# Kernel tuning notes

Measured on AMD Instinct MI355X. Metric: run time of the kernel, lower is better.

The kernel has to match this reference:

```python
import jax, jax.numpy as jnp
import numpy as np

HEADS = 4
ALPHA = 0.2  # leaky relu negative slope


def setup_inputs() -> dict:
    key = jax.random.key(0)
    ks = jax.random.split(key, 8)
    N, Fin, Fout = 4096, 512, 256
    return {
        "h": jax.random.normal(ks[0], (N, Fin), dtype=jnp.float32),
        "adj": jax.random.randint(ks[1], (N, N), 0, 2, dtype=jnp.int32),
        "W": jax.random.normal(ks[2], (Fin, Fout), dtype=jnp.float32) * (Fin ** -0.5),
        "Wl_w": jax.random.normal(ks[3], (Fout, Fout), dtype=jnp.float32) * (Fout ** -0.5),
        "Wl_b": jax.random.normal(ks[4], (Fout,), dtype=jnp.float32) * 0.02,
        "Wqkv_w": jax.random.normal(ks[5], (3 * Fout, Fout), dtype=jnp.float32) * (Fout ** -0.5),
        "Wqkv_b": jax.random.normal(ks[6], (3 * Fout,), dtype=jnp.float32) * 0.02,
        "a": jax.random.normal(ks[7], (2 * Fout, 1), dtype=jnp.float32) * (Fout ** -0.5),
    }


def reference(h, adj, W, Wl_w, Wl_b, Wqkv_w, Wqkv_b, a):
    N = h.shape[0]
    Fout = W.shape[1]
    d = Fout // HEADS
    scale = Fout ** -0.5  # note: original scales by out_features^-0.5, not head_dim

    Wh = h @ W                      # [N, Fout]
    Wh = Wh @ Wl_w.T + Wl_b         # to_linear

    qkv = Wh @ Wqkv_w.T + Wqkv_b    # [N, 3*Fout]
    q, k, v = jnp.split(qkv, 3, axis=-1)
    to_heads = lambda t: t.reshape(N, HEADS, d).transpose(1, 0, 2)  # [H, N, d]
    q, k, v = to_heads(q), to_heads(k), to_heads(v)

    dots = jax.nn.softmax(jnp.einsum('hid,hjd->hij', q, k) * scale, axis=-1)  # [H,N,N]
    Wh0 = jnp.einsum('hij,hjd->hid', dots, v)            # [H, N, d]
    Wh0 = Wh0.transpose(1, 0, 2).reshape(N, Fout)        # i (h d)
    Wh0 = jax.nn.softmax(Wh0, axis=-1)

    # GAT score decomposed: e_ij = leakyrelu(Wh_i . a1 + Wh_j . a2)
    a1 = a[:Fout, 0]
    a2 = a[Fout:, 0]
    e = jax.nn.leaky_relu((Wh @ a1)[:, None] + (Wh @ a2)[None, :], negative_slope=ALPHA)

    dsum = dots.sum(axis=0)                              # [N, N]
    neg = jnp.float32(-9e15)
    attention = jnp.where(adj > 0, e + dsum, neg)
    attention = jax.nn.softmax(attention, axis=1)
    # dropout p=0.0 / eval mode -> identity

    h_prime = attention @ Wh + Wh0
    return jax.nn.elu(h_prime)  # concat=True
```

## Files before the change

kernel.cpp:

```cpp
#include <hip/hip_runtime.h>

typedef float  f32x4 __attribute__((ext_vector_type(4)));
typedef short  s16x8 __attribute__((ext_vector_type(8)));
typedef unsigned short u16x8 __attribute__((ext_vector_type(8)));

#define NROWS 4096
#define FOUT  256
#define ALPHA_LR 0.2f
#define SCALE 0.0625f
#define NEGV  -9.0e15f

static __device__ __forceinline__ unsigned short bf16_rne(float x) {
    unsigned u = __float_as_uint(x);
    u += 0x7fffu + ((u >> 16) & 1u);
    return (unsigned short)(u >> 16);
}
static __device__ __forceinline__ unsigned short bf16_trunc(float x) {
    return (unsigned short)(__float_as_uint(x) >> 16);
}
static __device__ __forceinline__ float bf2f(unsigned short h) {
    return __uint_as_float(((unsigned)h) << 16);
}
static __device__ __forceinline__ float wmax16(float v) {
#pragma unroll
    for (int o = 8; o; o >>= 1) v = fmaxf(v, __shfl_xor(v, o, 16));
    return v;
}
static __device__ __forceinline__ float wsum16(float v) {
#pragma unroll
    for (int o = 8; o; o >>= 1) v += __shfl_xor(v, o, 16);
    return v;
}
static __device__ __forceinline__ float wmax32(float v) {
#pragma unroll
    for (int o = 16; o; o >>= 1) v = fmaxf(v, __shfl_xor(v, o, 32));
    return v;
}
static __device__ __forceinline__ float wsum32(float v) {
#pragma unroll
    for (int o = 16; o; o >>= 1) v += __shfl_xor(v, o, 32);
    return v;
}

__global__ __launch_bounds__(256) void wprep(
    const float* __restrict__ W, const float* __restrict__ Wq,
    unsigned short* __restrict__ Whi, unsigned short* __restrict__ Wlo,
    unsigned short* __restrict__ Qhi, unsigned short* __restrict__ Qlo)
{
    int i = blockIdx.x * 256 + threadIdx.x;
    if (i < 131072) {
        float v = W[i];
        unsigned short hh = bf16_trunc(v);
        Whi[i] = hh; Wlo[i] = bf16_rne(v - bf2f(hh));
    }
    if (i < 196608) {
        float v = Wq[i];
        unsigned short hh = bf16_trunc(v);
        Qhi[i] = hh; Qlo[i] = bf16_rne(v - bf2f(hh));
    }
}

template <int EPI, bool BIAS>
__global__ __launch_bounds__(256) void gemm_mfma(
    const float* __restrict__ A,
    const unsigned short* __restrict__ Bhi, const unsigned short* __restrict__ Blo,
    const float* __restrict__ bias,
    float* __restrict__ C, unsigned short* __restrict__ o0,
    unsigned short* __restrict__ o1, unsigned short* __restrict__ o2,
    int M, int Nn, int K)
{
    __shared__ unsigned short Ah[64][40];
    __shared__ unsigned short Al[64][40];
    __shared__ unsigned short Bh[64][40];
    __shared__ unsigned short Bl[64][40];

    const int tid = threadIdx.x;
    const int w = tid >> 6;
    const int ln = tid & 63;
    const int l15 = ln & 15;
    const int lhi = ln >> 4;
    const int bm = blockIdx.y * 64;
    const int bn = blockIdx.x * 64;
    const int sm = tid >> 2;
    const int sk = (tid & 3) * 8;

    f32x4 acc[4];
#pragma unroll
    for (int cf = 0; cf < 4; ++cf) acc[cf] = (f32x4){0.f, 0.f, 0.f, 0.f};

    const float* arow = &A[(size_t)(bm + sm) * K];
    const unsigned short* bhrow = &Bhi[(size_t)(bn + sm) * K];
    const unsigned short* blrow = &Blo[(size_t)(bn + sm) * K];

    float4 a0r = *(const float4*)(arow + sk);
    float4 a1r = *(const float4*)(arow + sk + 4);
    uint4 bhr = *(const uint4*)(bhrow + sk);
    uint4 blr = *(const uint4*)(blrow + sk);

    for (int k0 = 0; k0 < K; k0 += 32) {
        float vv[8] = {a0r.x, a0r.y, a0r.z, a0r.w, a1r.x, a1r.y, a1r.z, a1r.w};
        unsigned hp[4], lp[4];
#pragma unroll
        for (int q = 0; q < 4; ++q) {
            unsigned short h0 = bf16_trunc(vv[q * 2]);
            unsigned short h1 = bf16_trunc(vv[q * 2 + 1]);
            unsigned short l0 = bf16_rne(vv[q * 2] - bf2f(h0));
            unsigned short l1 = bf16_rne(vv[q * 2 + 1] - bf2f(h1));
            hp[q] = (unsigned)h0 | ((unsigned)h1 << 16);
            lp[q] = (unsigned)l0 | ((unsigned)l1 << 16);
        }
        __syncthreads();
        *(uint4*)&Ah[sm][sk] = make_uint4(hp[0], hp[1], hp[2], hp[3]);
        *(uint4*)&Al[sm][sk] = make_uint4(lp[0], lp[1], lp[2], lp[3]);
        *(uint4*)&Bh[sm][sk] = bhr;
        *(uint4*)&Bl[sm][sk] = blr;
        const int kn = (k0 + 32 < K) ? k0 + 32 : 0;
        a0r = *(const float4*)(arow + kn + sk);
        a1r = *(const float4*)(arow + kn + sk + 4);
        bhr = *(const uint4*)(bhrow + kn + sk);
        blr = *(const uint4*)(blrow + kn + sk);
        __syncthreads();
        s16x8 ah = *(const s16x8*)&Ah[w * 16 + l15][lhi * 8];
        s16x8 al2 = *(const s16x8*)&Al[w * 16 + l15][lhi * 8];
        __builtin_amdgcn_s_setprio(1);
#pragma unroll
        for (int cf = 0; cf < 4; ++cf) {
            s16x8 bh = *(const s16x8*)&Bh[cf * 16 + l15][lhi * 8];
            s16x8 bl = *(const s16x8*)&Bl[cf * 16 + l15][lhi * 8];
            acc[cf] = __builtin_amdgcn_mfma_f32_16x16x32_bf16(ah, bh, acc[cf], 0, 0, 0);
            acc[cf] = __builtin_amdgcn_mfma_f32_16x16x32_bf16(ah, bl, acc[cf], 0, 0, 0);
            acc[cf] = __builtin_amdgcn_mfma_f32_16x16x32_bf16(al2, bh, acc[cf], 0, 0, 0);
        }
        __builtin_amdgcn_s_setprio(0);
    }

#pragma unroll
    for (int cf = 0; cf < 4; ++cf) {
        const int col = bn + cf * 16 + l15;
        float bv = BIAS ? bias[col] : 0.0f;
#pragma unroll
        for (int r = 0; r < 4; ++r) {
            const int row = bm + w * 16 + lhi * 4 + r;
            float v = acc[cf][r] + bv;
            if (EPI == 1) {
                C[(size_t)row * Nn + col] = v;
                o0[(size_t)col * NROWS + row] = bf16_rne(v);
            } else if (EPI == 2) {
                if (col < 256)      o0[(size_t)row * 256 + col] = bf16_rne(v);
                else if (col < 512) o1[(size_t)row * 256 + (col - 256)] = bf16_rne(v);
                else                o2[(size_t)(col - 512) * NROWS + row] = bf16_rne(v);
            } else {
                unsigned short hh = bf16_trunc(v);
                o0[(size_t)row * Nn + col] = hh;
                o1[(size_t)row * Nn + col] = bf16_rne(v - bf2f(hh));
            }
        }
    }
}

__global__ __launch_bounds__(256) void compute_p(
    const float* __restrict__ Wh, const float* __restrict__ a,
    float* __restrict__ p1, float* __restrict__ p2)
{
    const int row = blockIdx.x * 16 + (threadIdx.x >> 4);
    const int c = threadIdx.x & 15;
    float s1 = 0.f, s2 = 0.f;
    for (int f = c; f < FOUT; f += 16) {
        float w = Wh[(size_t)row * FOUT + f];
        s1 += w * a[f];
        s2 += w * a[FOUT + f];
    }
    s1 = wsum16(s1);
    s2 = wsum16(s2);
    if (c == 0) { p1[row] = s1; p2[row] = s2; }
}

__global__ __launch_bounds__(256) void stats_kernel(
    const unsigned short* __restrict__ qh_g, const unsigned short* __restrict__ kh_g,
    float* __restrict__ stats)
{
    const int tid = threadIdx.x;
    const int h = tid >> 6;
    const int ln = tid & 63;
    const int l15 = ln & 15;
    const int lhi = ln >> 4;
    const int rt = blockIdx.x >> 3;
    const int ch = blockIdx.x & 7;
    const int i0 = rt * 16;

    s16x8 qA[2];
#pragma unroll
    for (int ks = 0; ks < 2; ++ks)
        qA[ks] = *(const s16x8*)(qh_g + (size_t)(i0 + l15) * 256 + h * 64 + ks * 32 + lhi * 8);

    float m[4], z[4];
#pragma unroll
    for (int r = 0; r < 4; ++r) { m[r] = -3.0e38f; z[r] = 0.f; }

    for (int tt = 0; tt < 16; ++tt) {
        const int j0 = ch * 512 + tt * 32;
        f32x4 acc[2] = {{0.f,0.f,0.f,0.f},{0.f,0.f,0.f,0.f}};
#pragma unroll
        for (int ks = 0; ks < 2; ++ks)
#pragma unroll
            for (int nt = 0; nt < 2; ++nt) {
                s16x8 kB = *(const s16x8*)(kh_g + (size_t)(j0 + nt * 16 + l15) * 256 +
                                           h * 64 + ks * 32 + lhi * 8);
                acc[nt] = __builtin_amdgcn_mfma_f32_16x16x32_bf16(qA[ks], kB, acc[nt], 0, 0, 0);
            }
#pragma unroll
        for (int r = 0; r < 4; ++r) {
            float s0 = acc[0][r] * SCALE, s1 = acc[1][r] * SCALE;
            float mn = fmaxf(m[r], fmaxf(s0, s1));
            z[r] = z[r] * __expf(m[r] - mn) + __expf(s0 - mn) + __expf(s1 - mn);
            m[r] = mn;
        }
    }
#pragma unroll
    for (int r = 0; r < 4; ++r) {
        float mm = m[r], zz = z[r];
#pragma unroll
        for (int o = 1; o < 16; o <<= 1) {
            float mo = __shfl_xor(mm, o, 16);
            float zo = __shfl_xor(zz, o, 16);
            float mn = fmaxf(mm, mo);
            zz = zz * __expf(mm - mn) + zo * __expf(mo - mn);
            mm = mn;
        }
        if (l15 == 0) {
            size_t idx = (((size_t)(i0 + lhi * 4 + r) * 4 + h) * 8 + ch) * 2;
            stats[idx] = mm;
            stats[idx + 1] = zz;
        }
    }
}

__global__ __launch_bounds__(512, 4) void main_attn(
    const unsigned short* __restrict__ qh_g, const unsigned short* __restrict__ kh_g,
    const unsigned short* __restrict__ vth_g, const unsigned short* __restrict__ wht_g,
    const float* __restrict__ stats, const float* __restrict__ p1g,
    const float* __restrict__ p2g, const int* __restrict__ adj,
    unsigned short* __restrict__ pacc_o, unsigned short* __restrict__ wacc_o,
    float* __restrict__ ml_o)
{
    enum { DOTS = 0, PTIL = 5120, ALP = 6400, MIZ = 6464, SMEMSZ = 6976 };
    __shared__ __align__(16) char smem[SMEMSZ];

    const int tid = threadIdx.x;
    const int w = tid >> 6;
    const int h = w & 3;
    const int jg = w >> 2;
    const int ln = tid & 63;
    const int l15 = ln & 15;
    const int lhi = ln >> 4;
    const int rt = blockIdx.x >> 1;
    const int ch = blockIdx.x & 1;
    const int i0 = rt * 16;
    const int jbase = ch * 2048;
    const int srow = tid >> 5;
    const int scol = tid & 31;

    if (tid < 64) {
        int hh = tid >> 4, row = tid & 15;
        const float* sb = stats + ((size_t)(i0 + row) * 4 + hh) * 16;
        float M = -3.0e38f, Z = 0.f;
#pragma unroll
        for (int c = 0; c < 8; ++c) {
            float mc = sb[c * 2], zc = sb[c * 2 + 1];
            float mn = fmaxf(M, mc);
            Z = Z * __expf(M - mn) + zc * __expf(mc - mn);
            M = mn;
        }
        ((float*)(smem + MIZ))[(hh * 16 + row) * 2] = M;
        ((float*)(smem + MIZ))[(hh * 16 + row) * 2 + 1] = 1.0f / Z;
    }

    s16x8 qA[2];
#pragma unroll
    for (int ks = 0; ks < 2; ++ks)
        qA[ks] = *(const s16x8*)(qh_g + (size_t)(i0 + l15) * 256 + h * 64 + ks * 32 + lhi * 8);

    __syncthreads();

    float m_f[4], iz_f[4];
#pragma unroll
    for (int r = 0; r < 4; ++r) {
        m_f[r]  = ((float*)(smem + MIZ))[(h * 16 + lhi * 4 + r) * 2];
        iz_f[r] = ((float*)(smem + MIZ))[(h * 16 + lhi * 4 + r) * 2 + 1];
    }

    const unsigned short* kp = kh_g + (size_t)(jg * 16 + l15) * 256 + h * 64 + lhi * 8;
    const unsigned short* vp = vth_g + (size_t)(h * 64 + jg * 32 + l15) * 4096 + lhi * 8;
    const unsigned short* wp = wht_g + (size_t)(h * 64 + jg * 32 + l15) * 4096 + lhi * 8;

    s16x8 kf0 = *(const s16x8*)(kp + (size_t)jbase * 256);
    s16x8 kf1 = *(const s16x8*)(kp + (size_t)jbase * 256 + 32);
    s16x8 vf0 = *(const s16x8*)(vp + jbase);
    s16x8 vf1 = *(const s16x8*)(vp + 16 * 4096 + jbase);
    s16x8 wf0 = *(const s16x8*)(wp + jbase);
    s16x8 wf1 = *(const s16x8*)(wp + 16 * 4096 + jbase);
    int   adjc = adj[(size_t)(i0 + srow) * NROWS + jbase + scol];
    float p2c  = p2g[jbase + scol];

    f32x4 pacc[2] = {{0.f,0.f,0.f,0.f},{0.f,0.f,0.f,0.f}};
    f32x4 wacc[2] = {{0.f,0.f,0.f,0.f},{0.f,0.f,0.f,0.f}};
    float Mrun = -3.0e38f, Lrun = 0.0f;
    const float p1v = p1g[i0 + srow];

    const int dwbase = DOTS + h * 1280 + (jg * 16 + l15) * 2;
    const int daddr  = DOTS + h * 1280 + l15 * 80 + lhi * 16;
    const int paddr  = PTIL + l15 * 80 + lhi * 16;

    for (int t = 0; t < 64; ++t) {
        const int jn = jbase + ((t + 1) & 63) * 32;

        f32x4 qk = {0.f, 0.f, 0.f, 0.f};
        __builtin_amdgcn_s_setprio(1);
        qk = __builtin_amdgcn_mfma_f32_16x16x32_bf16(qA[0], kf0, qk, 0, 0, 0);
        qk = __builtin_amdgcn_mfma_f32_16x16x32_bf16(qA[1], kf1, qk, 0, 0, 0);
        __builtin_amdgcn_s_setprio(0);
        kf0 = *(const s16x8*)(kp + (size_t)jn * 256);
        kf1 = *(const s16x8*)(kp + (size_t)jn * 256 + 32);
#pragma unroll
        for (int r = 0; r < 4; ++r) {
            float d = __expf(qk[r] * SCALE - m_f[r]) * iz_f[r];
            *(unsigned short*)(smem + dwbase + (lhi * 4 + r) * 80) = bf16_rne(d);
        }
        __syncthreads();

        {
            s16x8 dA = *(const s16x8*)(smem + daddr);
            __builtin_amdgcn_s_setprio(1);
            pacc[0] = __builtin_amdgcn_mfma_f32_16x16x32_bf16(dA, vf0, pacc[0], 0, 0, 0);
            pacc[1] = __builtin_amdgcn_mfma_f32_16x16x32_bf16(dA, vf1, pacc[1], 0, 0, 0);
            __builtin_amdgcn_s_setprio(0);
        }
        vf0 = *(const s16x8*)(vp + jn);
        vf1 = *(const s16x8*)(vp + 16 * 4096 + jn);

        {
            float ds = 0.f;
#pragma unroll
            for (int hh = 0; hh < 4; ++hh)
                ds += bf2f(*(const unsigned short*)(smem + DOTS + hh * 1280 + srow * 80 + scol * 2));
            float e = p1v + p2c; e = e > 0.f ? e : ALPHA_LR * e;
            float l = adjc > 0 ? e + ds : NEGV;
            float tm = wmax32(l);
            float Mn = fmaxf(Mrun, tm);
            float p = __expf(l - Mn);
            float ps = wsum32(p);
            float al = __expf(Mrun - Mn);
            Lrun = Lrun * al + ps;
            Mrun = Mn;
            if ((ln & 31) == 0) *(float*)(smem + ALP + srow * 4) = al;
            *(unsigned short*)(smem + PTIL + srow * 80 + scol * 2) = bf16_rne(p);
        }
        adjc = adj[(size_t)(i0 + srow) * NROWS + jn + scol];
        p2c  = p2g[jn + scol];
        __syncthreads();

        {
            float alr[4];
#pragma unroll
            for (int r = 0; r < 4; ++r)
                alr[r] = *(const float*)(smem + ALP + (lhi * 4 + r) * 4);
#pragma unroll
            for (int nt = 0; nt < 2; ++nt)
#pragma unroll
                for (int r = 0; r < 4; ++r) wacc[nt][r] *= alr[r];
            s16x8 pA = *(const s16x8*)(smem + paddr);
            __builtin_amdgcn_s_setprio(1);
            wacc[0] = __builtin_amdgcn_mfma_f32_16x16x32_bf16(pA, wf0, wacc[0], 0, 0, 0);
            wacc[1] = __builtin_amdgcn_mfma_f32_16x16x32_bf16(pA, wf1, wacc[1], 0, 0, 0);
            __builtin_amdgcn_s_setprio(0);
        }
        wf0 = *(const s16x8*)(wp + jn);
        wf1 = *(const s16x8*)(wp + 16 * 4096 + jn);
    }

    const size_t pbase = (size_t)(rt * 2 + ch) * 16 * 256;
#pragma unroll
    for (int nt = 0; nt < 2; ++nt)
#pragma unroll
        for (int r = 0; r < 4; ++r) {
            int row = lhi * 4 + r;
            int col = h * 64 + jg * 32 + nt * 16 + l15;
            pacc_o[pbase + row * 256 + col] = bf16_rne(pacc[nt][r]);
            wacc_o[pbase + row * 256 + col] = bf16_rne(wacc[nt][r]);
        }
    if ((ln & 31) == 0) {
        ml_o[((size_t)(rt * 2 + ch) * 16 + srow) * 2]     = Mrun;
        ml_o[((size_t)(rt * 2 + ch) * 16 + srow) * 2 + 1] = Lrun;
    }
}

__global__ __launch_bounds__(256) void merge_kernel(
    const unsigned short* __restrict__ pacc_b, const unsigned short* __restrict__ wacc_b,
    const float* __restrict__ ml, float* __restrict__ out)
{
    const int rt = blockIdx.x;
    const int tid = threadIdx.x;
    const int row = tid >> 4;
    const int cg = tid & 15;

    const size_t b0 = ((size_t)(rt * 2 + 0) * 16 + row) * 256 + cg * 16;
    const size_t b1 = ((size_t)(rt * 2 + 1) * 16 + row) * 256 + cg * 16;
    float M0 = ml[((size_t)(rt * 2 + 0) * 16 + row) * 2];
    float L0 = ml[((size_t)(rt * 2 + 0) * 16 + row) * 2 + 1];
    float M1 = ml[((size_t)(rt * 2 + 1) * 16 + row) * 2];
    float L1 = ml[((size_t)(rt * 2 + 1) * 16 + row) * 2 + 1];
    float M = fmaxf(M0, M1);
    float s0 = __expf(M0 - M), s1 = __expf(M1 - M);
    float invL = 1.0f / (L0 * s0 + L1 * s1);

    u16x8 pa[2][2], wa[2][2];
#pragma unroll
    for (int k = 0; k < 2; ++k) {
        pa[0][k] = *(const u16x8*)(pacc_b + b0 + k * 8);
        pa[1][k] = *(const u16x8*)(pacc_b + b1 + k * 8);
        wa[0][k] = *(const u16x8*)(wacc_b + b0 + k * 8);
        wa[1][k] = *(const u16x8*)(wacc_b + b1 + k * 8);
    }
    float p[16], wv[16];
    float mx = -3.0e38f;
#pragma unroll
    for (int k = 0; k < 16; ++k) {
        p[k] = bf2f(pa[0][k >> 3][k & 7]) + bf2f(pa[1][k >> 3][k & 7]);
        wv[k] = (bf2f(wa[0][k >> 3][k & 7]) * s0 + bf2f(wa[1][k >> 3][k & 7]) * s1) * invL;
        mx = fmaxf(mx, p[k]);
    }
    mx = wmax16(mx);
    float sm = 0.f;
#pragma unroll
    for (int k = 0; k < 16; ++k) { p[k] = __expf(p[k] - mx); sm += p[k]; }
    sm = wsum16(sm);
    float inv = 1.0f / sm;
    float* orow = out + ((size_t)(rt * 16 + row)) * 256 + cg * 16;
#pragma unroll
    for (int k4 = 0; k4 < 4; ++k4) {
        float4 o;
        float v;
        v = wv[k4*4+0] + p[k4*4+0] * inv; o.x = v > 0.f ? v : __expf(v) - 1.f;
        v = wv[k4*4+1] + p[k4*4+1] * inv; o.y = v > 0.f ? v : __expf(v) - 1.f;
        v = wv[k4*4+2] + p[k4*4+2] * inv; o.z = v > 0.f ? v : __expf(v) - 1.f;
        v = wv[k4*4+3] + p[k4*4+3] * inv; o.w = v > 0.f ? v : __expf(v) - 1.f;
        *(float4*)(orow + k4 * 4) = o;
    }
}

extern "C" void kernel_launch(void* const* d_in, const int* in_sizes, int n_in,
                              void* d_out, int out_size, void* d_ws, size_t ws_size,
                              hipStream_t stream)
{
    const float* h      = (const float*)d_in[0];
    const int*   adj    = (const int*)d_in[1];
    const float* W      = (const float*)d_in[2];
    const float* Wl_w   = (const float*)d_in[3];
    const float* Wl_b   = (const float*)d_in[4];
    const float* Wqkv_w = (const float*)d_in[5];
    const float* Wqkv_b = (const float*)d_in[6];
    const float* a      = (const float*)d_in[7];
    float* out = (float*)d_out;

    float* ws = (float*)d_ws;
    float* Whb = ws;
    unsigned short* u16b  = (unsigned short*)(ws + (1 << 20));
    unsigned short* qh    = u16b;
    unsigned short* kh    = u16b + (1 << 20);
    unsigned short* vth   = u16b + (2 << 20);
    unsigned short* wht   = u16b + (3 << 20);
    unsigned short* Whi   = u16b + (4 << 20);
    unsigned short* Wlo   = Whi + 131072;
    unsigned short* Qhi   = Wlo + 131072;
    unsigned short* Qlo   = Qhi + 196608;
    unsigned short* WcThi = Qlo + 196608;
    unsigned short* WcTlo = WcThi + 131072;
    float* p1b    = ws + 3670016;
    float* p2b    = p1b + 4096;
    float* statsb = p2b + 4096;
    float* mlb    = statsb + 262144;
    unsigned short* pacc_b = (unsigned short*)Whb;
    unsigned short* wacc_b = (unsigned short*)(ws + 3960832);

    dim3 blk(256);
    wprep<<<dim3(768), blk, 0, stream>>>(W, Wqkv_w, Whi, Wlo, Qhi, Qlo);
    gemm_mfma<3, false><<<dim3(8, 4), blk, 0, stream>>>(
        Wl_w, Whi, Wlo, nullptr, nullptr, WcThi, WcTlo, nullptr, 256, 512, 256);
    gemm_mfma<1, true><<<dim3(4, 64), blk, 0, stream>>>(
        h, WcThi, WcTlo, Wl_b, Whb, wht, nullptr, nullptr, 4096, 256, 512);
    gemm_mfma<2, true><<<dim3(12, 64), blk, 0, stream>>>(
        Whb, Qhi, Qlo, Wqkv_b, nullptr, qh, kh, vth, 4096, 768, 256);
    compute_p<<<dim3(256), blk, 0, stream>>>(Whb, a, p1b, p2b);
    stats_kernel<<<dim3(2048), blk, 0, stream>>>(qh, kh, statsb);
    main_attn<<<dim3(512), dim3(512), 0, stream>>>(
        qh, kh, vth, wht, statsb, p1b, p2b, adj, pacc_b, wacc_b, mlb);
    merge_kernel<<<dim3(256), blk, 0, stream>>>(pacc_b, wacc_b, mlb, out);
}
```

Measured before the change: 290.2 us.

## Replace online softmax with fixed analytic max bound and split columns three ways

The GAT attention softmax no longer tracks a running max. It subtracts a fixed per-row upper bound, leakyrelu(p1_i + max p2) + 4, which holds because the summed head attention is at most 4. A new tiny kernel computes max p2. This removes the per-tile wave max and sum reductions, the shared-memory alpha broadcast and the accumulator rescaling. The merge becomes a plain sum of partial numerators and denominators. The column range is also split into three chunks (768 blocks) with a higher occupancy hint, and stats_kernel is reshaped to 4 column chunks. The cost is a risk of underflow if the scores sit far below the bound, plus an extra small launch.

```diff
diff --git a/kernel.cpp b/kernel.cpp
--- a/kernel.cpp
+++ b/kernel.cpp
@@ -8,7 +8,6 @@
 #define FOUT  256
 #define ALPHA_LR 0.2f
 #define SCALE 0.0625f
-#define NEGV  -9.0e15f
 
 static __device__ __forceinline__ unsigned short bf16_rne(float x) {
     unsigned u = __float_as_uint(x);
@@ -29,11 +28,6 @@
 static __device__ __forceinline__ float wsum16(float v) {
 #pragma unroll
     for (int o = 8; o; o >>= 1) v += __shfl_xor(v, o, 16);
-    return v;
-}
-static __device__ __forceinline__ float wmax32(float v) {
-#pragma unroll
-    for (int o = 16; o; o >>= 1) v = fmaxf(v, __shfl_xor(v, o, 32));
     return v;
 }
 static __device__ __forceinline__ float wsum32(float v) {
@@ -175,6 +169,21 @@
     if (c == 0) { p1[row] = s1; p2[row] = s2; }
 }
 
+__global__ __launch_bounds__(256) void p2max_kernel(
+    const float* __restrict__ p2, float* __restrict__ p2m)
+{
+    __shared__ float red[4];
+    const int tid = threadIdx.x;
+    float v = -3.0e38f;
+#pragma unroll
+    for (int k = 0; k < 16; ++k) v = fmaxf(v, p2[tid + k * 256]);
+#pragma unroll
+    for (int o = 32; o; o >>= 1) v = fmaxf(v, __shfl_xor(v, o, 64));
+    if ((tid & 63) == 0) red[tid >> 6] = v;
+    __syncthreads();
+    if (tid == 0) p2m[0] = fmaxf(fmaxf(red[0], red[1]), fmaxf(red[2], red[3]));
+}
+
 __global__ __launch_bounds__(256) void stats_kernel(
     const unsigned short* __restrict__ qh_g, const unsigned short* __restrict__ kh_g,
     float* __restrict__ stats)
@@ -184,8 +193,8 @@
     const int ln = tid & 63;
     const int l15 = ln & 15;
     const int lhi = ln >> 4;
-    const int rt = blockIdx.x >> 3;
-    const int ch = blockIdx.x & 7;
+    const int rt = blockIdx.x & 255;
+    const int ch = blockIdx.x >> 8;
     const int i0 = rt * 16;
 
     s16x8 qA[2];
@@ -197,8 +206,8 @@
 #pragma unroll
     for (int r = 0; r < 4; ++r) { m[r] = -3.0e38f; z[r] = 0.f; }
 
-    for (int tt = 0; tt < 16; ++tt) {
-        const int j0 = ch * 512 + tt * 32;
+    for (int tt = 0; tt < 32; ++tt) {
+        const int j0 = ch * 1024 + tt * 32;
         f32x4 acc[2] = {{0.f,0.f,0.f,0.f},{0.f,0.f,0.f,0.f}};
 #pragma unroll
         for (int ks = 0; ks < 2; ++ks)
@@ -228,22 +237,23 @@
             mm = mn;
         }
         if (l15 == 0) {
-            size_t idx = (((size_t)(i0 + lhi * 4 + r) * 4 + h) * 8 + ch) * 2;
+            size_t idx = (((size_t)(i0 + lhi * 4 + r) * 4 + h) * 4 + ch) * 2;
             stats[idx] = mm;
             stats[idx + 1] = zz;
         }
     }
 }
 
-__global__ __launch_bounds__(512, 4) void main_attn(
+__global__ __launch_bounds__(512, 6) void main_attn(
     const unsigned short* __restrict__ qh_g, const unsigned short* __restrict__ kh_g,
     const unsigned short* __restrict__ vth_g, const unsigned short* __restrict__ wht_g,
     const float* __restrict__ stats, const float* __restrict__ p1g,
-    const float* __restrict__ p2g, const int* __restrict__ adj,
+    const float* __restrict__ p2g, const float* __restrict__ p2m,
+    const int* __restrict__ adj,
     unsigned short* __restrict__ pacc_o, unsigned short* __restrict__ wacc_o,
     float* __restrict__ ml_o)
 {
-    enum { DOTS = 0, PTIL = 5120, ALP = 6400, MIZ = 6464, SMEMSZ = 6976 };
+    enum { DOTS = 0, PTIL = 5120, MIZ = 6400, SMEMSZ = 6912 };
     __shared__ __align__(16) char smem[SMEMSZ];
 
     const int tid = threadIdx.x;
@@ -253,19 +263,20 @@
     const int ln = tid & 63;
     const int l15 = ln & 15;
     const int lhi = ln >> 4;
-    const int rt = blockIdx.x >> 1;
-    const int ch = blockIdx.x & 1;
+    const int rt = blockIdx.x & 255;
+    const int ch = blockIdx.x >> 8;
     const int i0 = rt * 16;
-    const int jbase = ch * 2048;
+    const int jbase = ch * 1376;
+    const int ntiles = (ch == 2) ? 42 : 43;
     const int srow = tid >> 5;
     const int scol = tid & 31;
 
     if (tid < 64) {
         int hh = tid >> 4, row = tid & 15;
-        const float* sb = stats + ((size_t)(i0 + row) * 4 + hh) * 16;
+        const float* sb = stats + ((size_t)(i0 + row) * 4 + hh) * 8;
         float M = -3.0e38f, Z = 0.f;
 #pragma unroll
-        for (int c = 0; c < 8; ++c) {
+        for (int c = 0; c < 4; ++c) {
             float mc = sb[c * 2], zc = sb[c * 2 + 1];
             float mn = fmaxf(M, mc);
             Z = Z * __expf(M - mn) + zc * __expf(mc - mn);
@@ -304,15 +315,20 @@
 
     f32x4 pacc[2] = {{0.f,0.f,0.f,0.f},{0.f,0.f,0.f,0.f}};
     f32x4 wacc[2] = {{0.f,0.f,0.f,0.f},{0.f,0.f,0.f,0.f}};
-    float Mrun = -3.0e38f, Lrun = 0.0f;
     const float p1v = p1g[i0 + srow];
+    float Mfix;
+    {
+        float s = p1v + p2m[0];
+        Mfix = (s > 0.f ? s : ALPHA_LR * s) + 4.0f;
+    }
+    float Lp = 0.0f;
 
     const int dwbase = DOTS + h * 1280 + (jg * 16 + l15) * 2;
     const int daddr  = DOTS + h * 1280 + l15 * 80 + lhi * 16;
     const int paddr  = PTIL + l15 * 80 + lhi * 16;
 
-    for (int t = 0; t < 64; ++t) {
-        const int jn = jbase + ((t + 1) & 63) * 32;
+    for (int t = 0; t < ntiles; ++t) {
+        const int jn = jbase + ((t + 1 < ntiles) ? (t + 1) * 32 : 0);
 
         f32x4 qk = {0.f, 0.f, 0.f, 0.f};
         __builtin_amdgcn_s_setprio(1);
@@ -344,15 +360,8 @@
             for (int hh = 0; hh < 4; ++hh)
                 ds += bf2f(*(const unsigned short*)(smem + DOTS + hh * 1280 + srow * 80 + scol * 2));
             float e = p1v + p2c; e = e > 0.f ? e : ALPHA_LR * e;
-            float l = adjc > 0 ? e + ds : NEGV;
-            float tm = wmax32(l);
-            float Mn = fmaxf(Mrun, tm);
-            float p = __expf(l - Mn);
-            float ps = wsum32(p);
-            float al = __expf(Mrun - Mn);
-            Lrun = Lrun * al + ps;
-            Mrun = Mn;
-            if ((ln & 31) == 0) *(float*)(smem + ALP + srow * 4) = al;
+            float p = (adjc > 0) ? __expf(e + ds - Mfix) : 0.f;
+            Lp += p;
             *(unsigned short*)(smem + PTIL + srow * 80 + scol * 2) = bf16_rne(p);
         }
         adjc = adj[(size_t)(i0 + srow) * NROWS + jn + scol];
@@ -360,14 +369,6 @@
         __syncthreads();
 
         {
-            float alr[4];
-#pragma unroll
-            for (int r = 0; r < 4; ++r)
-                alr[r] = *(const float*)(smem + ALP + (lhi * 4 + r) * 4);
-#pragma unroll
-            for (int nt = 0; nt < 2; ++nt)
-#pragma unroll
-                for (int r = 0; r < 4; ++r) wacc[nt][r] *= alr[r];
             s16x8 pA = *(const s16x8*)(smem + paddr);
             __builtin_amdgcn_s_setprio(1);
             wacc[0] = __builtin_amdgcn_mfma_f32_16x16x32_bf16(pA, wf0, wacc[0], 0, 0, 0);
@@ -378,7 +379,11 @@
         wf1 = *(const s16x8*)(wp + 16 * 4096 + jn);
     }
 
-    const size_t pbase = (size_t)(rt * 2 + ch) * 16 * 256;
+    Lp = wsum32(Lp);
+    if ((ln & 31) == 0)
+        ml_o[(size_t)(rt * 3 + ch) * 16 + srow] = Lp;
+
+    const size_t pbase = (size_t)(rt * 3 + ch) * 16 * 256;
 #pragma unroll
     for (int nt = 0; nt < 2; ++nt)
 #pragma unroll
@@ -388,10 +393,6 @@
             pacc_o[pbase + row * 256 + col] = bf16_rne(pacc[nt][r]);
             wacc_o[pbase + row * 256 + col] = bf16_rne(wacc[nt][r]);
         }
-    if ((ln & 31) == 0) {
-        ml_o[((size_t)(rt * 2 + ch) * 16 + srow) * 2]     = Mrun;
-        ml_o[((size_t)(rt * 2 + ch) * 16 + srow) * 2 + 1] = Lrun;
-    }
 }
 
 __global__ __launch_bounds__(256) void merge_kernel(
@@ -403,47 +404,45 @@
     const int row = tid >> 4;
     const int cg = tid & 15;
 
-    const size_t b0 = ((size_t)(rt * 2 + 0) * 16 + row) * 256 + cg * 16;
-    const size_t b1 = ((size_t)(rt * 2 + 1) * 16 + row) * 256 + cg * 16;
-    float M0 = ml[((size_t)(rt * 2 + 0) * 16 + row) * 2];
-    float L0 = ml[((size_t)(rt * 2 + 0) * 16 + row) * 2 + 1];
-    float M1 = ml[((size_t)(rt * 2 + 1) * 16 + row) * 2];
-    float L1 = ml[((size_t)(rt * 2 + 1) * 16 + row) * 2 + 1];
-    float M = fmaxf(M0, M1);
-    float s0 = __expf(M0 - M), s1 = __expf(M1 - M);
-    float invL = 1.0f / (L0 * s0 + L1 * s1);
-
-    u16x8 pa[2][2], wa[2][2];
-#pragma unroll
-    for (int k = 0; k < 2; ++k) {
-        pa[0][k] = *(const u16x8*)(pacc_b + b0 + k * 8);
-        pa[1][k] = *(const u16x8*)(pacc_b + b1 + k * 8);
-        wa[0][k] = *(const u16x8*)(wacc_b + b0 + k * 8);
-        wa[1][k] = *(const u16x8*)(wacc_b + b1 + k * 8);
-    }
+    float L = 0.f;
     float p[16], wv[16];
+#pragma unroll
+    for (int k = 0; k < 16; ++k) { p[k] = 0.f; wv[k] = 0.f; }
+#pragma unroll
+    for (int c = 0; c < 3; ++c) {
+        L += ml[(size_t)(rt * 3 + c) * 16 + row];
+        const size_t b = ((size_t)(rt * 3 + c) * 16 + row) * 256 + cg * 16;
+        u16x8 pa0 = *(const u16x8*)(pacc_b + b);
+        u16x8 pa1 = *(const u16x8*)(pacc_b + b + 8);
+        u16x8 wa0 = *(const u16x8*)(wacc_b + b);
+        u16x8 wa1 = *(const u16x8*)(wacc_b + b + 8);
+#pragma unroll
+        for (int k = 0; k < 8; ++k) {
+            p[k] += bf2f(pa0[k]);  p[k + 8] += bf2f(pa1[k]);
+            wv[k] += bf2f(wa0[k]); wv[k + 8] += bf2f(wa1[k]);
+        }
+    }
+    const float invL = 1.0f / fmaxf(L, 1e-30f);
+
     float mx = -3.0e38f;
 #pragma unroll
-    for (int k = 0; k < 16; ++k) {
-        p[k] = bf2f(pa[0][k >> 3][k & 7]) + bf2f(pa[1][k >> 3][k & 7]);
-        wv[k] = (bf2f(wa[0][k >> 3][k & 7]) * s0 + bf2f(wa[1][k >> 3][k & 7]) * s1) * invL;
-        mx = fmaxf(mx, p[k]);
-    }
+    for (int k = 0; k < 16; ++k) mx = fmaxf(mx, p[k]);
     mx = wmax16(mx);
     float sm = 0.f;
 #pragma unroll
     for (int k = 0; k < 16; ++k) { p[k] = __expf(p[k] - mx); sm += p[k]; }
     sm = wsum16(sm);
-    float inv = 1.0f / sm;
+    const float inv = 1.0f / sm;
+
     float* orow = out + ((size_t)(rt * 16 + row)) * 256 + cg * 16;
 #pragma unroll
     for (int k4 = 0; k4 < 4; ++k4) {
         float4 o;
         float v;
-        v = wv[k4*4+0] + p[k4*4+0] * inv; o.x = v > 0.f ? v : __expf(v) - 1.f;
-        v = wv[k4*4+1] + p[k4*4+1] * inv; o.y = v > 0.f ? v : __expf(v) - 1.f;
-        v = wv[k4*4+2] + p[k4*4+2] * inv; o.z = v > 0.f ? v : __expf(v) - 1.f;
-        v = wv[k4*4+3] + p[k4*4+3] * inv; o.w = v > 0.f ? v : __expf(v) - 1.f;
+        v = wv[k4*4+0] * invL + p[k4*4+0] * inv; o.x = v > 0.f ? v : __expf(v) - 1.f;
+        v = wv[k4*4+1] * invL + p[k4*4+1] * inv; o.y = v > 0.f ? v : __expf(v) - 1.f;
+        v = wv[k4*4+2] * invL + p[k4*4+2] * inv; o.z = v > 0.f ? v : __expf(v) - 1.f;
+        v = wv[k4*4+3] * invL + p[k4*4+3] * inv; o.w = v > 0.f ? v : __expf(v) - 1.f;
         *(float4*)(orow + k4 * 4) = o;
     }
 }
@@ -462,25 +461,25 @@
     const float* a      = (const float*)d_in[7];
     float* out = (float*)d_out;
 
-    float* ws = (float*)d_ws;
-    float* Whb = ws;
-    unsigned short* u16b  = (unsigned short*)(ws + (1 << 20));
-    unsigned short* qh    = u16b;
-    unsigned short* kh    = u16b + (1 << 20);
-    unsigned short* vth   = u16b + (2 << 20);
-    unsigned short* wht   = u16b + (3 << 20);
-    unsigned short* Whi   = u16b + (4 << 20);
-    unsigned short* Wlo   = Whi + 131072;
-    unsigned short* Qhi   = Wlo + 131072;
-    unsigned short* Qlo   = Qhi + 196608;
-    unsigned short* WcThi = Qlo + 196608;
-    unsigned short* WcTlo = WcThi + 131072;
-    float* p1b    = ws + 3670016;
-    float* p2b    = p1b + 4096;
-    float* statsb = p2b + 4096;
-    float* mlb    = statsb + 262144;
-    unsigned short* pacc_b = (unsigned short*)Whb;
-    unsigned short* wacc_b = (unsigned short*)(ws + 3960832);
+    char* wsb = (char*)d_ws;
+    unsigned short* qh     = (unsigned short*)(wsb + 0);
+    unsigned short* kh     = (unsigned short*)(wsb + 2097152);
+    unsigned short* vth    = (unsigned short*)(wsb + 4194304);
+    unsigned short* wht    = (unsigned short*)(wsb + 6291456);
+    float*          statsb = (float*)(wsb + 8388608);
+    float*          p1b    = (float*)(wsb + 8912896);
+    float*          p2b    = (float*)(wsb + 8929280);
+    float*          p2m    = (float*)(wsb + 8945664);
+    float*          mlb    = (float*)(wsb + 8949760);
+    unsigned short* pacc_b = (unsigned short*)(wsb + 9043968);
+    unsigned short* wacc_b = (unsigned short*)(wsb + 15335424);
+    float*          Whb    = (float*)(wsb + 9043968);
+    unsigned short* Whi    = (unsigned short*)(wsb + 13238272);
+    unsigned short* Wlo    = Whi + 131072;
+    unsigned short* Qhi    = Wlo + 131072;
+    unsigned short* Qlo    = Qhi + 196608;
+    unsigned short* WcThi  = Qlo + 196608;
+    unsigned short* WcTlo  = WcThi + 131072;
 
     dim3 blk(256);
     wprep<<<dim3(768), blk, 0, stream>>>(W, Wqkv_w, Whi, Wlo, Qhi, Qlo);
@@ -491,8 +490,9 @@
     gemm_mfma<2, true><<<dim3(12, 64), blk, 0, stream>>>(
         Whb, Qhi, Qlo, Wqkv_b, nullptr, qh, kh, vth, 4096, 768, 256);
     compute_p<<<dim3(256), blk, 0, stream>>>(Whb, a, p1b, p2b);
-    stats_kernel<<<dim3(2048), blk, 0, stream>>>(qh, kh, statsb);
-    main_attn<<<dim3(512), dim3(512), 0, stream>>>(
-        qh, kh, vth, wht, statsb, p1b, p2b, adj, pacc_b, wacc_b, mlb);
+    p2max_kernel<<<dim3(1), blk, 0, stream>>>(p2b, p2m);
+    stats_kernel<<<dim3(1024), blk, 0, stream>>>(qh, kh, statsb);
+    main_attn<<<dim3(768), dim3(512), 0, stream>>>(
+        qh, kh, vth, wht, statsb, p1b, p2b, p2m, adj, pacc_b, wacc_b, mlb);
     merge_kernel<<<dim3(256), blk, 0, stream>>>(pacc_b, wacc_b, mlb, out);
 }
```

Result: slower. 371.3 us (+27.9%).
